# Kernel optimization log

Hardware: AMD Instinct MI355X
Metric: run time of the kernel (lower is better)

Reference implementation:

```python
import jax, jax.numpy as jnp
import numpy as np

EPS = 1e-5

def gn(x, gamma, beta):
    # GroupNorm(num_groups=1) on [N, C]: normalize over channel dim per row
    m = x.mean(-1, keepdims=True)
    v = ((x - m) ** 2).mean(-1, keepdims=True)
    return (x - m) * jax.lax.rsqrt(v + EPS) * gamma + beta

def setup_inputs() -> dict:
    key = jax.random.key(0)
    N, M, E, D = 50000, 50000, 500000, 128
    ks = jax.random.split(key, 32)
    s = 0.05
    inp = {
        'agts': jax.random.normal(ks[0], (N, D), jnp.float32),
        'ctx': jax.random.normal(ks[1], (M, D), jnp.float32),
        'agt_ctrs': jax.random.normal(ks[2], (N, 2), jnp.float32),
        'ctx_ctrs': jax.random.normal(ks[3], (M, 2), jnp.float32),
        'hi': jax.random.randint(ks[4], (E,), 0, N, jnp.int32),
        'wi': jax.random.randint(ks[5], (E,), 0, M, jnp.int32),
        # dist MLP: Linear(2,D,bias) -> ReLU -> Linear(D,D,nobias)+GN+ReLU
        'W_d1': jax.random.normal(ks[6], (2, D), jnp.float32) * s,
        'b_d1': jnp.zeros((D,), jnp.float32),
        'W_d2': jax.random.normal(ks[7], (D, D), jnp.float32) * s,
        'g_d2': jnp.ones((D,), jnp.float32),
        'b_d2': jnp.zeros((D,), jnp.float32),
        # query: Linear(D,D,nobias)+GN+ReLU
        'W_q': jax.random.normal(ks[8], (D, D), jnp.float32) * s,
        'g_q': jnp.ones((D,), jnp.float32),
        'b_q': jnp.zeros((D,), jnp.float32),
        # ctx MLP: Linear(3D,D,nobias)+GN+ReLU -> Linear(D,D,nobias)
        'W_c1': jax.random.normal(ks[9], (3 * D, D), jnp.float32) * s,
        'g_c1': jnp.ones((D,), jnp.float32),
        'b_c1': jnp.zeros((D,), jnp.float32),
        'W_c2': jax.random.normal(ks[10], (D, D), jnp.float32) * s,
        # agt linear (nobias), post-scatter GN, final Linear(D,D,nobias)+GN (no act)
        'W_a': jax.random.normal(ks[11], (D, D), jnp.float32) * s,
        'g_n': jnp.ones((D,), jnp.float32),
        'b_n': jnp.zeros((D,), jnp.float32),
        'W_l': jax.random.normal(ks[12], (D, D), jnp.float32) * s,
        'g_l': jnp.ones((D,), jnp.float32),
        'b_l': jnp.zeros((D,), jnp.float32),
    }
    return inp

def reference(agts, ctx, agt_ctrs, ctx_ctrs, hi, wi,
              W_d1, b_d1, W_d2, g_d2, b_d2,
              W_q, g_q, b_q,
              W_c1, g_c1, b_c1, W_c2,
              W_a, g_n, b_n, W_l, g_l, b_l):
    res = agts
    # gather per-edge relative distances and embed
    dist = agt_ctrs[hi] - ctx_ctrs[wi]                      # [E, 2]
    d = jax.nn.relu(dist @ W_d1 + b_d1)                     # [E, D]
    d = jax.nn.relu(gn(d @ W_d2, g_d2, b_d2))               # [E, D]
    # per-edge agent query
    q = jax.nn.relu(gn(agts[hi] @ W_q, g_q, b_q))           # [E, D]
    # concat(dist_emb, query, gathered ctx) -> message MLP
    msg = jnp.concatenate([d, q, ctx[wi]], axis=-1)         # [E, 3D]
    msg = jax.nn.relu(gn(msg @ W_c1, g_c1, b_c1)) @ W_c2    # [E, D]
    # transform agents and scatter-add messages
    a = agts @ W_a
    a = a.at[hi].add(msg)
    a = jax.nn.relu(gn(a, g_n, b_n))
    a = gn(a @ W_l, g_l, b_l)   # act=False
    a = jax.nn.relu(a + res)
    return a
```

## Files before the change

### kernel.cpp

```cpp
#include <hip/hip_runtime.h>
#include <hip/hip_bf16.h>
#include <stdint.h>


typedef __bf16 bfx8 __attribute__((ext_vector_type(8)));
typedef float f32x4 __attribute__((ext_vector_type(4)));
typedef short s16x2 __attribute__((ext_vector_type(2)));

__device__ __forceinline__ unsigned short f2bfu(float f) {
  unsigned u = __builtin_bit_cast(unsigned, f);
  return (unsigned short)((u + 0x7fffu + ((u >> 16) & 1u)) >> 16);
}
__device__ __forceinline__ float bfu2f(unsigned short u) {
  return __builtin_bit_cast(float, ((unsigned)u) << 16);
}
__device__ __forceinline__ unsigned pk2(unsigned x, unsigned y) {
  float lo = bfu2f((unsigned short)(x & 0xffffu)) + bfu2f((unsigned short)(y & 0xffffu));
  float hi = bfu2f((unsigned short)(x >> 16)) + bfu2f((unsigned short)(y >> 16));
  return (unsigned)f2bfu(lo) | ((unsigned)f2bfu(hi) << 16);
}

__device__ __forceinline__ void atomAddBf2(unsigned short* p, unsigned v) {
#if defined(__has_builtin) && __has_builtin(__builtin_amdgcn_global_atomic_fadd_v2bf16)
  __builtin_amdgcn_global_atomic_fadd_v2bf16(
      (__attribute__((address_space(1))) s16x2*)p, __builtin_bit_cast(s16x2, v));
#else
  unsigned* q = (unsigned*)p;
  unsigned old = *q;
  while (true) {
    unsigned nv = pk2(old, v);
    unsigned prev = atomicCAS(q, old, nv);
    if (prev == old) break;
    old = prev;
  }
#endif
}

__device__ __forceinline__ int swzb(int row, int kbyte) {
  return (row * 256 + kbyte) ^ ((row & 7) << 4);
}

__device__ __forceinline__ void stage_w(const unsigned short* wsrc, char* dst, int tid, int nth) {
  const uint4* s = (const uint4*)wsrc;
  uint4* d = (uint4*)dst;
  for (int i = tid; i < 2048; i += nth) d[i] = s[i];
}

template <bool A_FROM_LDS>
__device__ __forceinline__ void wave_gemm(const char* WtL, const char* XL,
                                          const bfx8* aF, f32x4 acc[8],
                                          int lg, int lr) {
#pragma unroll
  for (int ks = 0; ks < 4; ++ks) {
    bfx8 a;
    if (A_FROM_LDS)
      a = *(const bfx8*)(XL + swzb(lr, (ks * 32 + lg * 8) * 2));
    else
      a = aF[ks];
#pragma unroll
    for (int t = 0; t < 8; ++t) {
      int n = t * 16 + lr;
      bfx8 b = *(const bfx8*)(WtL + swzb(n, (ks * 32 + lg * 8) * 2));
      acc[t] = __builtin_amdgcn_mfma_f32_16x16x32_bf16(a, b, acc[t], 0, 0, 0);
    }
  }
}

__device__ __forceinline__ void wave_gn(f32x4 acc[8], const float* g, const float* b,
                                        int lg, int lr, bool do_relu) {
  float s0 = 0.f, s1 = 0.f, s2 = 0.f, s3 = 0.f;
  float q0 = 0.f, q1 = 0.f, q2 = 0.f, q3 = 0.f;
#pragma unroll
  for (int t = 0; t < 8; ++t) {
    float v0 = acc[t][0], v1 = acc[t][1], v2 = acc[t][2], v3 = acc[t][3];
    s0 += v0; q0 += v0 * v0;
    s1 += v1; q1 += v1 * v1;
    s2 += v2; q2 += v2 * v2;
    s3 += v3; q3 += v3 * v3;
  }
#pragma unroll
  for (int m = 1; m <= 8; m <<= 1) {
    s0 += __shfl_xor(s0, m, 64); q0 += __shfl_xor(q0, m, 64);
    s1 += __shfl_xor(s1, m, 64); q1 += __shfl_xor(q1, m, 64);
    s2 += __shfl_xor(s2, m, 64); q2 += __shfl_xor(q2, m, 64);
    s3 += __shfl_xor(s3, m, 64); q3 += __shfl_xor(q3, m, 64);
  }
  float gc[8], bc[8];
#pragma unroll
  for (int t = 0; t < 8; ++t) { gc[t] = g[t * 16 + lr]; bc[t] = b[t * 16 + lr]; }
  float mean[4], rstd[4];
  {
    const float inv = 1.f / 128.f;
    float m0 = s0 * inv, m1 = s1 * inv, m2 = s2 * inv, m3 = s3 * inv;
    mean[0] = m0; mean[1] = m1; mean[2] = m2; mean[3] = m3;
    rstd[0] = rsqrtf(q0 * inv - m0 * m0 + 1e-5f);
    rstd[1] = rsqrtf(q1 * inv - m1 * m1 + 1e-5f);
    rstd[2] = rsqrtf(q2 * inv - m2 * m2 + 1e-5f);
    rstd[3] = rsqrtf(q3 * inv - m3 * m3 + 1e-5f);
  }
#pragma unroll
  for (int t = 0; t < 8; ++t) {
#pragma unroll
    for (int r = 0; r < 4; ++r) {
      float v = (acc[t][r] - mean[r]) * rstd[r] * gc[t] + bc[t];
      if (do_relu) v = fmaxf(v, 0.f);
      acc[t][r] = v;
    }
  }
}

__device__ __forceinline__ void wave_stage(char* XL, const f32x4 acc[8], int lg, int lr) {
#pragma unroll
  for (int t = 0; t < 8; ++t) {
#pragma unroll
    for (int r = 0; r < 4; ++r) {
      int row = 4 * lg + r, c = t * 16 + lr;
      *(unsigned short*)(XL + swzb(row, 2 * c)) = f2bfu(acc[t][r]);
    }
  }
}

__global__ void k_prep_weights(const float* Wd2, const float* Wc1, const float* Wc2,
                               const float* Wq, const float* Wa, const float* Wl,
                               unsigned short* wsW) {
  __shared__ unsigned short tmp[128 * 128];
  int m = blockIdx.x;
  const float* src;
  switch (m) {
    case 0: src = Wd2; break;
    case 1: src = Wc1; break;
    case 2: src = Wc1 + 128 * 128; break;
    case 3: src = Wc1 + 256 * 128; break;
    case 4: src = Wc2; break;
    case 5: src = Wq; break;
    case 6: src = Wa; break;
    default: src = Wl; break;
  }
  int tid = threadIdx.x;
#pragma unroll
  for (int i = 0; i < 16; ++i) {
    int lin = i * 256 + tid;
    float4 v = ((const float4*)src)[lin];
    ushort4 b;
    b.x = f2bfu(v.x); b.y = f2bfu(v.y); b.z = f2bfu(v.z); b.w = f2bfu(v.w);
    *(ushort4*)&tmp[lin * 4] = b;
  }
  __syncthreads();
  unsigned short* dst = wsW + (size_t)m * 16384;
#pragma unroll
  for (int i = 0; i < 16; ++i) {
    int lin = i * 256 + tid;
    int n = lin >> 5, q = lin & 31, k0 = q * 4;
    ushort4 b;
    b.x = tmp[(k0 + 0) * 128 + n];
    b.y = tmp[(k0 + 1) * 128 + n];
    b.z = tmp[(k0 + 2) * 128 + n];
    b.w = tmp[(k0 + 3) * 128 + n];
    *(ushort4*)((char*)dst + swzb(n, k0 * 2)) = b;
  }
}

__global__ __launch_bounds__(256, 2) void k_ctx(const float* ctx, const unsigned short* wsW,
                                                unsigned short* cc, int M) {
  __shared__ __align__(16) char lds[32768];
  int tid = threadIdx.x, wid = tid >> 6, lane = tid & 63, lg = lane >> 4, lr = lane & 15;
  int base = blockIdx.x * 64;
  stage_w(wsW + 3 * 16384, lds, tid, 256);
  int row = base + 16 * wid + lr;
  int rload = row < M ? row : M - 1;
  bfx8 cf[4];
#pragma unroll
  for (int ks = 0; ks < 4; ++ks) {
    int k0 = ks * 32 + lg * 8;
    const float4* p = (const float4*)&ctx[(size_t)rload * 128 + k0];
    float4 a = p[0], b = p[1];
    bfx8 f;
    f[0] = (__bf16)a.x; f[1] = (__bf16)a.y; f[2] = (__bf16)a.z; f[3] = (__bf16)a.w;
    f[4] = (__bf16)b.x; f[5] = (__bf16)b.y; f[6] = (__bf16)b.z; f[7] = (__bf16)b.w;
    cf[ks] = f;
  }
  __syncthreads();
  f32x4 acc[8];
#pragma unroll
  for (int t = 0; t < 8; ++t) acc[t] = 0.f;
  wave_gemm<false>(lds, nullptr, cf, acc, lg, lr);
#pragma unroll
  for (int r = 0; r < 4; ++r) {
    int grow = base + 16 * wid + 4 * lg + r;
    if (grow < M) {
#pragma unroll
      for (int t = 0; t < 8; ++t)
        cc[(size_t)grow * 128 + t * 16 + lr] = f2bfu(acc[t][r]);
    }
  }
}

__global__ __launch_bounds__(768, 3) void k_agents(const float* agts, const float* g_q,
                                                   const float* b_q, const unsigned short* wsW,
                                                   unsigned short* qc, int N) {
  __shared__ __align__(16) char lds[114688];
  char* WqL = lds;
  char* WcL = lds + 32768;
  int tid = threadIdx.x, wid = tid >> 6, lane = tid & 63, lg = lane >> 4, lr = lane & 15;
  char* actL = lds + 65536 + wid * 4096;
  stage_w(wsW + 5 * 16384, WqL, tid, 768);
  stage_w(wsW + 2 * 16384, WcL, tid, 768);
  __syncthreads();
  int nTiles = (N + 15) >> 4;
  int stride = gridDim.x * 12;
  for (int tile = blockIdx.x * 12 + wid; tile < nTiles; tile += stride) {
    int base = tile << 4;
    int row = base + lr; if (row >= N) row = N - 1;
    bfx8 af[4];
#pragma unroll
    for (int ks = 0; ks < 4; ++ks) {
      int k0 = ks * 32 + lg * 8;
      const float4* p = (const float4*)&agts[(size_t)row * 128 + k0];
      float4 a = p[0], b = p[1];
      bfx8 f;
      f[0] = (__bf16)a.x; f[1] = (__bf16)a.y; f[2] = (__bf16)a.z; f[3] = (__bf16)a.w;
      f[4] = (__bf16)b.x; f[5] = (__bf16)b.y; f[6] = (__bf16)b.z; f[7] = (__bf16)b.w;
      af[ks] = f;
    }
    f32x4 acc[8];
#pragma unroll
    for (int t = 0; t < 8; ++t) acc[t] = 0.f;
    wave_gemm<false>(WqL, nullptr, af, acc, lg, lr);
    wave_gn(acc, g_q, b_q, lg, lr, true);
    wave_stage(actL, acc, lg, lr);
#pragma unroll
    for (int t = 0; t < 8; ++t) acc[t] = 0.f;
    wave_gemm<true>(WcL, actL, nullptr, acc, lg, lr);
#pragma unroll
    for (int r = 0; r < 4; ++r) {
      int grow = base + 4 * lg + r;
      if (grow < N) {
#pragma unroll
        for (int t = 0; t < 8; ++t)
          qc[(size_t)grow * 128 + t * 16 + lr] = f2bfu(acc[t][r]);
      }
    }
  }
}

__global__ __launch_bounds__(768, 3) void k_edge(
    const float* agt_ctrs, const float* ctx_ctrs, const int* hi, const int* wi,
    const float* W_d1, const float* b_d1, const float* g_d2, const float* b_d2,
    const float* g_c1, const float* b_c1, const unsigned short* wsW,
    const unsigned short* qc, const unsigned short* cc, unsigned short* S, int E) {
  __shared__ __align__(16) char lds[163840];
  char* Wd2L = lds;
  char* Wc1L = lds + 32768;
  int tid = threadIdx.x, wid = tid >> 6, lane = tid & 63, lg = lane >> 4, lr = lane & 15;
  char* QCCL = lds + 65536 + wid * 8192;
  char* actL = QCCL + 4096;
  stage_w(wsW + 0 * 16384, Wd2L, tid, 768);
  stage_w(wsW + 1 * 16384, Wc1L, tid, 768);
  __syncthreads();
  int nTiles = (E + 15) >> 4;
  int stride = gridDim.x * 12;
  for (int tile = blockIdx.x * 12 + wid; tile < nTiles; tile += stride) {
    int base = tile << 4;
    {
      int gr = lane >> 2, gq = lane & 3;
      int ge = base + gr; if (ge >= E) ge = E - 1;
      int gh = hi[ge], gw2 = wi[ge];
      const uint4* qrow = (const uint4*)(qc + (size_t)gh * 128) + gq * 4;
      const uint4* crow = (const uint4*)(cc + (size_t)gw2 * 128) + gq * 4;
#pragma unroll
      for (int i = 0; i < 4; ++i) {
        uint4 av = qrow[i], bv = crow[i];
        uint4 o;
        o.x = pk2(av.x, bv.x); o.y = pk2(av.y, bv.y);
        o.z = pk2(av.z, bv.z); o.w = pk2(av.w, bv.w);
        *(uint4*)(QCCL + swzb(gr, gq * 64 + i * 16)) = o;
      }
    }
    bfx8 d1f[4];
    {
      int e1 = base + lr; if (e1 >= E) e1 = E - 1;
      int h1 = hi[e1], w1 = wi[e1];
      float dx = agt_ctrs[2 * h1] - ctx_ctrs[2 * w1];
      float dy = agt_ctrs[2 * h1 + 1] - ctx_ctrs[2 * w1 + 1];
#pragma unroll
      for (int ks = 0; ks < 4; ++ks) {
        int k0 = ks * 32 + lg * 8;
        const float4* w0 = (const float4*)&W_d1[k0];
        const float4* w1p = (const float4*)&W_d1[128 + k0];
        const float4* bp = (const float4*)&b_d1[k0];
        float4 w0a = w0[0], w0b = w0[1];
        float4 w1a = w1p[0], w1b = w1p[1];
        float4 ba = bp[0], bb = bp[1];
        bfx8 f;
        f[0] = (__bf16)fmaxf(dx * w0a.x + dy * w1a.x + ba.x, 0.f);
        f[1] = (__bf16)fmaxf(dx * w0a.y + dy * w1a.y + ba.y, 0.f);
        f[2] = (__bf16)fmaxf(dx * w0a.z + dy * w1a.z + ba.z, 0.f);
        f[3] = (__bf16)fmaxf(dx * w0a.w + dy * w1a.w + ba.w, 0.f);
        f[4] = (__bf16)fmaxf(dx * w0b.x + dy * w1b.x + bb.x, 0.f);
        f[5] = (__bf16)fmaxf(dx * w0b.y + dy * w1b.y + bb.y, 0.f);
        f[6] = (__bf16)fmaxf(dx * w0b.z + dy * w1b.z + bb.z, 0.f);
        f[7] = (__bf16)fmaxf(dx * w0b.w + dy * w1b.w + bb.w, 0.f);
        d1f[ks] = f;
      }
    }
    f32x4 acc[8];
#pragma unroll
    for (int t = 0; t < 8; ++t) acc[t] = 0.f;
    wave_gemm<false>(Wd2L, nullptr, d1f, acc, lg, lr);
    wave_gn(acc, g_d2, b_d2, lg, lr, true);
    wave_stage(actL, acc, lg, lr);
#pragma unroll
    for (int t = 0; t < 8; ++t) {
#pragma unroll
      for (int r = 0; r < 4; ++r)
        acc[t][r] = bfu2f(*(const unsigned short*)(QCCL + swzb(4 * lg + r, 2 * (16 * t + lr))));
    }
    wave_gemm<true>(Wc1L, actL, nullptr, acc, lg, lr);
    wave_gn(acc, g_c1, b_c1, lg, lr, true);
    int hh[4], valid[4];
#pragma unroll
    for (int r = 0; r < 4; ++r) {
      int er = base + 4 * lg + r;
      valid[r] = er < E;
      hh[r] = hi[valid[r] ? er : 0];
    }
    bool evn = (lane & 1) == 0;
#pragma unroll
    for (int t = 0; t < 8; ++t) {
      bool mine = evn ? (t < 4) : (t >= 4);
#pragma unroll
      for (int r = 0; r < 4; ++r) {
        float v = acc[t][r];
        float vx = __shfl_xor(v, 1, 64);
        if (mine && valid[r]) {
          unsigned pkv = evn ? ((unsigned)f2bfu(v) | ((unsigned)f2bfu(vx) << 16))
                             : ((unsigned)f2bfu(vx) | ((unsigned)f2bfu(v) << 16));
          int col = (16 * t + lr) & ~1;
          atomAddBf2(S + (size_t)hh[r] * 128 + col, pkv);
        }
      }
    }
  }
}

__global__ __launch_bounds__(768, 3) void k_final(const float* agts, const float* g_n,
                                                  const float* b_n, const float* g_l,
                                                  const float* b_l, const unsigned short* wsW,
                                                  const unsigned short* S, float* out, int N) {
  __shared__ __align__(16) char lds[147456];
  char* WaL = lds;
  char* Wc2L = lds + 32768;
  char* WlL = lds + 65536;
  int tid = threadIdx.x, wid = tid >> 6, lane = tid & 63, lg = lane >> 4, lr = lane & 15;
  char* actL = lds + 98304 + wid * 4096;
  stage_w(wsW + 6 * 16384, WaL, tid, 768);
  stage_w(wsW + 4 * 16384, Wc2L, tid, 768);
  stage_w(wsW + 7 * 16384, WlL, tid, 768);
  __syncthreads();
  int nTiles = (N + 15) >> 4;
  int stride = gridDim.x * 12;
  for (int tile = blockIdx.x * 12 + wid; tile < nTiles; tile += stride) {
    int base = tile << 4;
    int row = base + lr; if (row >= N) row = N - 1;
    bfx8 af[4], sf[4];
#pragma unroll
    for (int ks = 0; ks < 4; ++ks) {
      int k0 = ks * 32 + lg * 8;
      const float4* p = (const float4*)&agts[(size_t)row * 128 + k0];
      float4 a = p[0], b = p[1];
      bfx8 f;
      f[0] = (__bf16)a.x; f[1] = (__bf16)a.y; f[2] = (__bf16)a.z; f[3] = (__bf16)a.w;
      f[4] = (__bf16)b.x; f[5] = (__bf16)b.y; f[6] = (__bf16)b.z; f[7] = (__bf16)b.w;
      af[ks] = f;
      sf[ks] = *(const bfx8*)&S[(size_t)row * 128 + k0];
    }
    f32x4 acc[8];
#pragma unroll
    for (int t = 0; t < 8; ++t) acc[t] = 0.f;
    wave_gemm<false>(WaL, nullptr, af, acc, lg, lr);
    wave_gemm<false>(Wc2L, nullptr, sf, acc, lg, lr);
    wave_gn(acc, g_n, b_n, lg, lr, true);
    wave_stage(actL, acc, lg, lr);
#pragma unroll
    for (int t = 0; t < 8; ++t) acc[t] = 0.f;
    wave_gemm<true>(WlL, actL, nullptr, acc, lg, lr);
    wave_gn(acc, g_l, b_l, lg, lr, false);
#pragma unroll
    for (int r = 0; r < 4; ++r) {
      int grow = base + 4 * lg + r;
      if (grow < N) {
#pragma unroll
        for (int t = 0; t < 8; ++t) {
          int c = t * 16 + lr;
          float res = agts[(size_t)grow * 128 + c];
          out[(size_t)grow * 128 + c] = fmaxf(acc[t][r] + res, 0.f);
        }
      }
    }
  }
}

extern "C" void kernel_launch(void* const* d_in, const int* in_sizes, int n_in,
                              void* d_out, int out_size, void* d_ws, size_t ws_size,
                              hipStream_t stream) {
  const float* agts = (const float*)d_in[0];
  const float* ctx = (const float*)d_in[1];
  const float* agt_ctrs = (const float*)d_in[2];
  const float* ctx_ctrs = (const float*)d_in[3];
  const int* hi = (const int*)d_in[4];
  const int* wi = (const int*)d_in[5];
  const float* W_d1 = (const float*)d_in[6];
  const float* b_d1 = (const float*)d_in[7];
  const float* W_d2 = (const float*)d_in[8];
  const float* g_d2 = (const float*)d_in[9];
  const float* b_d2 = (const float*)d_in[10];
  const float* W_q = (const float*)d_in[11];
  const float* g_q = (const float*)d_in[12];
  const float* b_q = (const float*)d_in[13];
  const float* W_c1 = (const float*)d_in[14];
  const float* g_c1 = (const float*)d_in[15];
  const float* b_c1 = (const float*)d_in[16];
  const float* W_c2 = (const float*)d_in[17];
  const float* W_a = (const float*)d_in[18];
  const float* g_n = (const float*)d_in[19];
  const float* b_n = (const float*)d_in[20];
  const float* W_l = (const float*)d_in[21];
  const float* g_l = (const float*)d_in[22];
  const float* b_l = (const float*)d_in[23];

  int N = in_sizes[0] / 128;
  int M = in_sizes[1] / 128;
  int E = in_sizes[4];

  float* out = (float*)d_out;
  char* ws = (char*)d_ws;
  unsigned short* qcP = (unsigned short*)ws;
  unsigned short* ccP = (unsigned short*)(ws + (size_t)N * 256);
  unsigned short* Sp = (unsigned short*)(ws + (size_t)N * 256 + (size_t)M * 256);
  unsigned short* wsW = (unsigned short*)(ws + (size_t)N * 512 + (size_t)M * 256);

  hipMemsetAsync(Sp, 0, (size_t)N * 256, stream);
  k_prep_weights<<<8, 256, 0, stream>>>(W_d2, W_c1, W_c2, W_q, W_a, W_l, wsW);
  k_ctx<<<(M + 63) / 64, 256, 0, stream>>>(ctx, wsW, ccP, M);
  k_agents<<<256, 768, 0, stream>>>(agts, g_q, b_q, wsW, qcP, N);
  k_edge<<<256, 768, 0, stream>>>(agt_ctrs, ctx_ctrs, hi, wi, W_d1, b_d1,
                                  g_d2, b_d2, g_c1, b_c1, wsW, qcP, ccP, Sp, E);
  k_final<<<256, 768, 0, stream>>>(agts, g_n, b_n, g_l, b_l, wsW, Sp, out, N);
}
```

Baseline: 336.7 us.

## Counting-sort edges by destination and segment-reduce messages before scatter

Adds histogram, single-block scan and fill kernels that bucket edges by destination agent (hi), and feeds the sorted index arrays to the edge kernel. Each wave now stages its 16 edge messages in LDS and sums runs of equal destination in fp32. It writes each run once with a plain store, using bf16x2 atomics only when the run crosses a tile boundary. This targets the per-edge global atomic traffic and improves locality of the agent-query gathers. In exchange it adds three extra launches, a serial single-block scan over N, and random atomics in the fill pass.

```diff
diff --git a/kernel.cpp b/kernel.cpp
--- a/kernel.cpp
+++ b/kernel.cpp
@@ -157,6 +157,44 @@
     b.z = tmp[(k0 + 2) * 128 + n];
     b.w = tmp[(k0 + 3) * 128 + n];
     *(ushort4*)((char*)dst + swzb(n, k0 * 2)) = b;
+  }
+}
+
+__global__ void k_hist(const int* hi, int* cnt, int E) {
+  int e = blockIdx.x * 256 + threadIdx.x;
+  if (e < E) atomicAdd(&cnt[hi[e]], 1);
+}
+
+__global__ __launch_bounds__(1024) void k_scan(const int* cnt, int* cur, int N) {
+  __shared__ int part[1024];
+  int tid = threadIdx.x;
+  int C = (N + 1023) >> 10;
+  int b0 = tid * C, b1 = b0 + C; if (b1 > N) b1 = N; if (b0 > N) b0 = N;
+  int s = 0;
+  for (int i = b0; i < b1; ++i) s += cnt[i];
+  part[tid] = s;
+  __syncthreads();
+  for (int d = 1; d < 1024; d <<= 1) {
+    int v = (tid >= d) ? part[tid - d] : 0;
+    __syncthreads();
+    part[tid] += v;
+    __syncthreads();
+  }
+  int excl = (tid == 0) ? 0 : part[tid - 1];
+  for (int i = b0; i < b1; ++i) {
+    cur[i] = excl;
+    excl += cnt[i];
+  }
+}
+
+__global__ void k_fill(const int* hi, const int* wi, int* cur,
+                       int* hi_s, int* wi_s, int E) {
+  int e = blockIdx.x * 256 + threadIdx.x;
+  if (e < E) {
+    int h = hi[e];
+    int p = atomicAdd(&cur[h], 1);
+    hi_s[p] = h;
+    wi_s[p] = wi[e];
   }
 }
 
@@ -244,7 +282,7 @@
 }
 
 __global__ __launch_bounds__(768, 3) void k_edge(
-    const float* agt_ctrs, const float* ctx_ctrs, const int* hi, const int* wi,
+    const float* agt_ctrs, const float* ctx_ctrs, const int* hi_s, const int* wi_s,
     const float* W_d1, const float* b_d1, const float* g_d2, const float* b_d2,
     const float* g_c1, const float* b_c1, const unsigned short* wsW,
     const unsigned short* qc, const unsigned short* cc, unsigned short* S, int E) {
@@ -252,8 +290,10 @@
   char* Wd2L = lds;
   char* Wc1L = lds + 32768;
   int tid = threadIdx.x, wid = tid >> 6, lane = tid & 63, lg = lane >> 4, lr = lane & 15;
-  char* QCCL = lds + 65536 + wid * 8192;
-  char* actL = QCCL + 4096;
+  char* region = lds + 65536 + wid * 8192;
+  char* QCCL = region;
+  char* actL = region + 4096;
+  float* hB = (float*)region;
   stage_w(wsW + 0 * 16384, Wd2L, tid, 768);
   stage_w(wsW + 1 * 16384, Wc1L, tid, 768);
   __syncthreads();
@@ -264,7 +304,7 @@
     {
       int gr = lane >> 2, gq = lane & 3;
       int ge = base + gr; if (ge >= E) ge = E - 1;
-      int gh = hi[ge], gw2 = wi[ge];
+      int gh = hi_s[ge], gw2 = wi_s[ge];
       const uint4* qrow = (const uint4*)(qc + (size_t)gh * 128) + gq * 4;
       const uint4* crow = (const uint4*)(cc + (size_t)gw2 * 128) + gq * 4;
 #pragma unroll
@@ -279,7 +319,7 @@
     bfx8 d1f[4];
     {
       int e1 = base + lr; if (e1 >= E) e1 = E - 1;
-      int h1 = hi[e1], w1 = wi[e1];
+      int h1 = hi_s[e1], w1 = wi_s[e1];
       float dx = agt_ctrs[2 * h1] - ctx_ctrs[2 * w1];
       float dy = agt_ctrs[2 * h1 + 1] - ctx_ctrs[2 * w1 + 1];
 #pragma unroll
@@ -317,26 +357,40 @@
     }
     wave_gemm<true>(Wc1L, actL, nullptr, acc, lg, lr);
     wave_gn(acc, g_c1, b_c1, lg, lr, true);
-    int hh[4], valid[4];
-#pragma unroll
-    for (int r = 0; r < 4; ++r) {
-      int er = base + 4 * lg + r;
-      valid[r] = er < E;
-      hh[r] = hi[valid[r] ? er : 0];
-    }
-    bool evn = (lane & 1) == 0;
 #pragma unroll
     for (int t = 0; t < 8; ++t) {
-      bool mine = evn ? (t < 4) : (t >= 4);
-#pragma unroll
-      for (int r = 0; r < 4; ++r) {
-        float v = acc[t][r];
-        float vx = __shfl_xor(v, 1, 64);
-        if (mine && valid[r]) {
-          unsigned pkv = evn ? ((unsigned)f2bfu(v) | ((unsigned)f2bfu(vx) << 16))
-                             : ((unsigned)f2bfu(vx) | ((unsigned)f2bfu(v) << 16));
-          int col = (16 * t + lr) & ~1;
-          atomAddBf2(S + (size_t)hh[r] * 128 + col, pkv);
+#pragma unroll
+      for (int r = 0; r < 4; ++r)
+        hB[(4 * lg + r) * 128 + 16 * t + lr] = acc[t][r];
+    }
+    {
+      int nprev = (base > 0) ? hi_s[base - 1] : -1;
+      int nnext = (base + 16 < E) ? hi_s[base + 16] : -1;
+      int curn = -1, seg_start = 0;
+      float s0 = 0.f, s1 = 0.f;
+#pragma unroll
+      for (int r = 0; r <= 16; ++r) {
+        int n;
+        if (r < 16) {
+          int sl = base + r;
+          n = (sl < E) ? hi_s[sl] : -1;
+        } else {
+          n = -2;
+        }
+        if (n != curn) {
+          if (curn >= 0) {
+            bool atomS = (seg_start == 0) && (curn == nprev);
+            bool atomE = (r == 16) && (curn == nnext);
+            unsigned pkv = (unsigned)f2bfu(s0) | ((unsigned)f2bfu(s1) << 16);
+            unsigned short* addr = S + (size_t)curn * 128 + 2 * lane;
+            if (atomS || atomE) atomAddBf2(addr, pkv);
+            else *(unsigned*)addr = pkv;
+          }
+          curn = n; seg_start = r; s0 = 0.f; s1 = 0.f;
+        }
+        if (r < 16 && n >= 0) {
+          float2 hv = *(const float2*)(hB + r * 128 + 2 * lane);
+          s0 += hv.x; s1 += hv.y;
         }
       }
     }
@@ -434,16 +488,25 @@
 
   float* out = (float*)d_out;
   char* ws = (char*)d_ws;
-  unsigned short* qcP = (unsigned short*)ws;
-  unsigned short* ccP = (unsigned short*)(ws + (size_t)N * 256);
-  unsigned short* Sp = (unsigned short*)(ws + (size_t)N * 256 + (size_t)M * 256);
-  unsigned short* wsW = (unsigned short*)(ws + (size_t)N * 512 + (size_t)M * 256);
-
+  size_t o = 0;
+  unsigned short* qcP = (unsigned short*)(ws + o); o += (size_t)N * 256;
+  unsigned short* ccP = (unsigned short*)(ws + o); o += (size_t)M * 256;
+  unsigned short* Sp  = (unsigned short*)(ws + o); o += (size_t)N * 256;
+  unsigned short* wsW = (unsigned short*)(ws + o); o += 262144;
+  int* cnt  = (int*)(ws + o); o += ((size_t)N * 4 + 255) & ~255ull;
+  int* cur  = (int*)(ws + o); o += ((size_t)N * 4 + 255) & ~255ull;
+  int* hi_s = (int*)(ws + o); o += ((size_t)E * 4 + 255) & ~255ull;
+  int* wi_s = (int*)(ws + o); o += ((size_t)E * 4 + 255) & ~255ull;
+
+  hipMemsetAsync(cnt, 0, (size_t)N * 4, stream);
   hipMemsetAsync(Sp, 0, (size_t)N * 256, stream);
   k_prep_weights<<<8, 256, 0, stream>>>(W_d2, W_c1, W_c2, W_q, W_a, W_l, wsW);
+  k_hist<<<(E + 255) / 256, 256, 0, stream>>>(hi, cnt, E);
+  k_scan<<<1, 1024, 0, stream>>>(cnt, cur, N);
+  k_fill<<<(E + 255) / 256, 256, 0, stream>>>(hi, wi, cur, hi_s, wi_s, E);
   k_ctx<<<(M + 63) / 64, 256, 0, stream>>>(ctx, wsW, ccP, M);
   k_agents<<<256, 768, 0, stream>>>(agts, g_q, b_q, wsW, qcP, N);
-  k_edge<<<256, 768, 0, stream>>>(agt_ctrs, ctx_ctrs, hi, wi, W_d1, b_d1,
+  k_edge<<<256, 768, 0, stream>>>(agt_ctrs, ctx_ctrs, hi_s, wi_s, W_d1, b_d1,
                                   g_d2, b_d2, g_c1, b_c1, wsW, qcP, ccP, Sp, E);
   k_final<<<256, 768, 0, stream>>>(agts, g_n, b_n, g_l, b_l, wsW, Sp, out, N);
 }
```

New measurement: 363.5 us. 1.08x slower.
